# Performance work log

Measured on AMD Instinct MI355X. Metric: run time of the kernel, lower is better.

The kernel has to match this reference:

```python
import jax, jax.numpy as jnp
import numpy as np

H = 128          # hidden_size
IN = 93          # input_size
NL = 4           # num_layers
B, T = 256, 512  # batch, seq_len


def setup_inputs() -> dict:
    key = jax.random.key(0)
    ks = jax.random.split(key, 8)
    s = 1.0 / np.sqrt(H)  # pytorch LSTM init range scale
    x = jax.random.normal(ks[0], (B, T, IN), jnp.float32)
    W_ih0 = jax.random.normal(ks[1], (4 * H, IN), jnp.float32) * s   # layer 0 input weights
    W_ih_rest = jax.random.normal(ks[2], (NL - 1, 4 * H, H), jnp.float32) * s  # layers 1..3
    W_hh = jax.random.normal(ks[3], (NL, 4 * H, H), jnp.float32) * s
    b_ih = jax.random.normal(ks[4], (NL, 4 * H), jnp.float32) * s
    b_hh = jax.random.normal(ks[5], (NL, 4 * H), jnp.float32) * s
    W_fc = jax.random.normal(ks[6], (1, H), jnp.float32) * s
    b_fc = jax.random.normal(ks[7], (1,), jnp.float32) * s
    return {"x": x, "W_ih0": W_ih0, "W_ih_rest": W_ih_rest, "W_hh": W_hh,
            "b_ih": b_ih, "b_hh": b_hh, "W_fc": W_fc, "b_fc": b_fc}


def _lstm_layer(x_tm, W_ih, W_hh_l, bi, bh):
    # x_tm: [T, B, in]; precompute input-side gates as one big GEMM
    gates_x = jnp.einsum('tbi,gi->tbg', x_tm, W_ih) + bi + bh  # [T,B,4H]

    def step(carry, gx):
        h, c = carry
        g = gx + h @ W_hh_l.T                      # [B,4H]
        i, f, gg, o = jnp.split(g, 4, axis=-1)     # pytorch gate order: i,f,g,o
        i = jax.nn.sigmoid(i)
        f = jax.nn.sigmoid(f)
        gg = jnp.tanh(gg)
        o = jax.nn.sigmoid(o)
        c = f * c + i * gg
        h = o * jnp.tanh(c)
        return (h, c), h

    b = x_tm.shape[1]
    h0 = jnp.zeros((b, H), x_tm.dtype)
    (_, _), hs = jax.lax.scan(step, (h0, h0), gates_x)
    return hs  # [T,B,H]


def reference(x, W_ih0, W_ih_rest, W_hh, b_ih, b_hh, W_fc, b_fc):
    # Eval-mode forward (dropout inactive), matching model.eval() semantics.
    h = jnp.transpose(x, (1, 0, 2))  # time-major [T,B,IN]
    h = _lstm_layer(h, W_ih0, W_hh[0], b_ih[0], b_hh[0])
    for l in range(1, NL):
        h = _lstm_layer(h, W_ih_rest[l - 1], W_hh[l], b_ih[l], b_hh[l])
    out = jax.nn.sigmoid(jnp.einsum('tbh,oh->tbo', h, W_fc) + b_fc)  # [T,B,1]
    return jnp.transpose(out, (1, 0, 2))  # [B,T,1]
```

## Files before the change

### kernel.cpp

```cpp
#include <hip/hip_runtime.h>
#include <hip/hip_bf16.h>

#define H_    128
#define IN_   93
#define NL_   4
#define B_    256
#define T_    512
#define G_    512
#define W_    32
#define LOG2E 1.44269504088896f

typedef __attribute__((ext_vector_type(8))) short bf16x8;
typedef __attribute__((ext_vector_type(4))) float f32x4;
typedef unsigned long long u64;

#define RING_SLOT (B_ * H_)
#define RING_L    ((size_t)W_ * RING_SLOT)

__device__ __forceinline__ ushort bf16_rn(float f) {
    uint x = __float_as_uint(f);
    uint r = (x + 0x7FFFu + ((x >> 16) & 1u)) >> 16;
    return (ushort)r;
}
__device__ __forceinline__ float exp2_fast(float x) { return __builtin_amdgcn_exp2f(x); }
__device__ __forceinline__ float rcp_fast(float x)  { return __builtin_amdgcn_rcpf(x); }

__device__ __forceinline__ int spin_ge(int* p, int target) {
    int v = __hip_atomic_load(p, __ATOMIC_ACQUIRE, __HIP_MEMORY_SCOPE_AGENT);
    while (v < target) {
        __builtin_amdgcn_s_sleep(2);
        v = __hip_atomic_load(p, __ATOMIC_ACQUIRE, __HIP_MEMORY_SCOPE_AGENT);
    }
    return v;
}

__global__ void prep_x(const float* __restrict__ x, ushort* __restrict__ xb) {
    int idx = blockIdx.x * 256 + threadIdx.x;
    int t = idx / (B_ * 96);
    int rem = idx % (B_ * 96);
    int b = rem / 96;
    int k = rem % 96;
    float v = 0.0f;
    if (k < IN_) v = x[((size_t)b * T_ + t) * IN_ + k];
    xb[idx] = bf16_rn(v);
}

__global__ void prep_w(const float* __restrict__ Wih0,
                       const float* __restrict__ Wihr,
                       const float* __restrict__ Whh,
                       ushort* __restrict__ Wc) {
    int idx = blockIdx.x * 256 + threadIdx.x;
    int l = idx / (G_ * 256);
    int rem = idx % (G_ * 256);
    int g = rem / 256;
    int k = rem % 256;
    int kx = (l == 0) ? 96 : 128;
    float v = 0.0f;
    if (k < kx) {
        if (l == 0) { if (k < IN_) v = Wih0[g * IN_ + k]; }
        else        { v = Wihr[(((size_t)(l - 1)) * G_ + g) * H_ + k]; }
    } else if (k < kx + H_) {
        v = Whh[(((size_t)l) * G_ + g) * H_ + (k - kx)];
    }
    float scale = (g >= 256 && g < 384) ? (2.0f * LOG2E) : LOG2E;
    Wc[idx] = bf16_rn(v * scale);
}

__global__ void prep_bias(const float* __restrict__ bih,
                          const float* __restrict__ bhh,
                          float* __restrict__ bc) {
    int idx = blockIdx.x * 256 + threadIdx.x;
    int g = idx & 511;
    float scale = (g >= 256 && g < 384) ? (2.0f * LOG2E) : LOG2E;
    bc[idx] = (bih[idx] + bhh[idx]) * scale;
}

__global__ void zero_prog(int* __restrict__ prog) {
    int i = threadIdx.x;
    for (int k = i; k < NL_ * 16 * 16; k += 256) prog[k] = 0;
}

__global__ __launch_bounds__(512, 2)
void recur_all(const ushort* __restrict__ xb,
               const ushort* __restrict__ Wc,
               const float* __restrict__ biasc,
               ushort* __restrict__ ring,
               ushort* __restrict__ h3,
               int* __restrict__ prog) {
    __shared__ ushort comb[2][16][272];

    const int bid = blockIdx.x;
    const int l = bid >> 4;
    const int g = bid & 15;
    const int kx = (l == 0) ? 96 : 128;

    const int tid = threadIdx.x;
    const int w   = tid >> 6;
    const int ln  = tid & 63;
    const int q   = ln >> 4;
    const int lo  = ln & 15;
    const int u   = (w << 4) | lo;
    const int b0  = g << 4;

    const ushort* Wl = Wc + (size_t)l * G_ * 256;
    const float*  bl = biasc + l * G_;
    int* prog_self = prog + (l * 16 + g) * 16;
    int* prog_up   = prog + ((l - 1) * 16 + g) * 16;
    int* prog_down = prog + ((l + 1) * 16 + g) * 16;

    ushort* ring_self = ring + (size_t)l * RING_L;
    const ushort* ring_up = ring + (size_t)(l - 1) * RING_L;

    for (int i = tid; i < 2 * 16 * 272; i += 512) ((ushort*)comb)[i] = 0;

    bf16x8 bw[4][8];
#pragma unroll
    for (int tu = 0; tu < 4; ++tu)
#pragma unroll
        for (int s = 0; s < 8; ++s) {
            const ushort* pp = Wl + ((size_t)((tu << 7) + u) << 8) + (s << 5) + (q << 3);
            bw[tu][s] = *(const bf16x8*)pp;
        }

    const float bv0 = bl[u];
    const float bv1 = bl[128 + u];
    const float bv2 = bl[256 + u];
    const float bv3 = bl[384 + u];

    f32x4 cc = {0.0f, 0.0f, 0.0f, 0.0f};

    const int crow = tid >> 5;
    const int cu4  = (tid & 31) << 2;
    const int seg  = tid & 31;
    const bool act = (seg < 24);

    uint2 xr = {0u, 0u};
    u64 hx = 0;
    int avail = 0;

    if (l == 0) {
        if (act) xr = *(const uint2*)(xb + (size_t)(b0 + crow) * 96 + (seg << 2));
    } else {
        avail = spin_ge(prog_up, (9 < T_) ? 9 : T_);
        hx = __hip_atomic_load((u64*)(ring_up + (size_t)(b0 + crow) * H_ + cu4),
                               __ATOMIC_RELAXED, __HIP_MEMORY_SCOPE_AGENT);
    }

    __syncthreads();

    for (int t = 0; t < T_; ++t) {
        const int p = t & 1;

        if (l == 0) {
            if (act) *(uint2*)&comb[p][crow][seg << 2] = xr;
        } else {
            *(u64*)&comb[p][crow][cu4] = hx;
        }

        __syncthreads();

        if (tid == 0 && t >= 1)
            __hip_atomic_store(prog_self, t - 1, __ATOMIC_RELAXED, __HIP_MEMORY_SCOPE_AGENT);

        if (t >= 1) {
            u64 hold = *(const u64*)&comb[p][crow][kx + cu4];
            if (l < 3) {
                u64* dst = (u64*)(ring_self + (size_t)((t - 1) & (W_ - 1)) * RING_SLOT +
                                  (size_t)(b0 + crow) * H_ + cu4);
                __hip_atomic_store(dst, hold, __ATOMIC_RELAXED, __HIP_MEMORY_SCOPE_AGENT);
            } else {
                *(u64*)(h3 + (size_t)(t - 1) * RING_SLOT + (size_t)(b0 + crow) * H_ + cu4) = hold;
            }
        }

        if (l < 3 && t >= 32 && (t & 15) == 0)
            (void)spin_ge(prog_down, t - 17);

        if (t < T_ - 1) {
            if (l == 0) {
                if (act) xr = *(const uint2*)(xb + (size_t)((t + 1) * B_ + b0 + crow) * 96 + (seg << 2));
            } else {
                if (avail < t + 2) {
                    int tgt = t + 9; if (tgt > T_) tgt = T_;
                    avail = spin_ge(prog_up, tgt);
                }
                hx = __hip_atomic_load((u64*)(ring_up + (size_t)((t + 1) & (W_ - 1)) * RING_SLOT +
                                              (size_t)(b0 + crow) * H_ + cu4),
                                       __ATOMIC_RELAXED, __HIP_MEMORY_SCOPE_AGENT);
            }
        }

        f32x4 a0 = {bv0, bv0, bv0, bv0};
        f32x4 a1 = {bv1, bv1, bv1, bv1};
        f32x4 a2 = {bv2, bv2, bv2, bv2};
        f32x4 a3 = {bv3, bv3, bv3, bv3};
#pragma unroll
        for (int s = 0; s < 8; ++s) {
            bf16x8 av = *(const bf16x8*)&comb[p][lo][(s << 5) + (q << 3)];
            a0 = __builtin_amdgcn_mfma_f32_16x16x32_bf16(av, bw[0][s], a0, 0, 0, 0);
            a1 = __builtin_amdgcn_mfma_f32_16x16x32_bf16(av, bw[1][s], a1, 0, 0, 0);
            a2 = __builtin_amdgcn_mfma_f32_16x16x32_bf16(av, bw[2][s], a2, 0, 0, 0);
            a3 = __builtin_amdgcn_mfma_f32_16x16x32_bf16(av, bw[3][s], a3, 0, 0, 0);
        }

#pragma unroll
        for (int r = 0; r < 4; ++r) {
            float ei = exp2_fast(fminf(-a0[r], 60.0f));
            float ef = exp2_fast(-a1[r]);
            float eg = exp2_fast(fminf(-a2[r], 60.0f));
            float eo = exp2_fast(fminf(-a3[r], 60.0f));
            float rf  = rcp_fast(1.0f + ef);
            float rig = rcp_fast((1.0f + ei) * (1.0f + eg));
            float cn  = __builtin_fmaf(cc[r], rf, (1.0f - eg) * rig);
            cc[r] = cn;
            float ec  = exp2_fast(fminf(-2.88539008177793f * cn, 60.0f));
            float roc = rcp_fast((1.0f + eo) * (1.0f + ec));
            float h_  = (1.0f - ec) * roc;
            comb[p ^ 1][(q << 2) + r][kx + u] = bf16_rn(h_);
        }
    }

    __syncthreads();
    {
        u64 hold = *(const u64*)&comb[T_ & 1][crow][kx + cu4];
        if (l < 3) {
            u64* dst = (u64*)(ring_self + (size_t)((T_ - 1) & (W_ - 1)) * RING_SLOT +
                              (size_t)(b0 + crow) * H_ + cu4);
            __hip_atomic_store(dst, hold, __ATOMIC_RELAXED, __HIP_MEMORY_SCOPE_AGENT);
        } else {
            *(u64*)(h3 + (size_t)(T_ - 1) * RING_SLOT + (size_t)(b0 + crow) * H_ + cu4) = hold;
        }
    }
    __syncthreads();
    if (tid == 0)
        __hip_atomic_store(prog_self, T_, __ATOMIC_RELAXED, __HIP_MEMORY_SCOPE_AGENT);
}

__global__ void fc_kernel(const ushort* __restrict__ h3,
                          const float* __restrict__ wfc,
                          const float* __restrict__ bfc,
                          float* __restrict__ out) {
    int t = blockIdx.x;
    int b = threadIdx.x;
    const uint4* hp = (const uint4*)(h3 + ((size_t)t * B_ + b) * H_);
    float acc = 0.0f;
#pragma unroll
    for (int kk = 0; kk < 16; ++kk) {
        uint4 pv = hp[kk];
        const uint vv[4] = {pv.x, pv.y, pv.z, pv.w};
#pragma unroll
        for (int j = 0; j < 4; ++j) {
            float f0 = __uint_as_float(vv[j] << 16);
            float f1 = __uint_as_float(vv[j] & 0xFFFF0000u);
            acc = __builtin_fmaf(f0, wfc[kk * 8 + j * 2 + 0], acc);
            acc = __builtin_fmaf(f1, wfc[kk * 8 + j * 2 + 1], acc);
        }
    }
    float z = acc + bfc[0];
    out[(size_t)b * T_ + t] = rcp_fast(1.0f + exp2_fast(-z * LOG2E));
}

extern "C" void kernel_launch(void* const* d_in, const int* in_sizes, int n_in,
                              void* d_out, int out_size, void* d_ws, size_t ws_size,
                              hipStream_t stream) {
    const float* x    = (const float*)d_in[0];
    const float* Wih0 = (const float*)d_in[1];
    const float* Wihr = (const float*)d_in[2];
    const float* Whh  = (const float*)d_in[3];
    const float* bih  = (const float*)d_in[4];
    const float* bhh  = (const float*)d_in[5];
    const float* Wfc  = (const float*)d_in[6];
    const float* bfc  = (const float*)d_in[7];
    float* out = (float*)d_out;

    char* ws = (char*)d_ws;
    const size_t xb_bytes   = (size_t)T_ * B_ * 96 * 2;
    const size_t wc_bytes   = (size_t)NL_ * G_ * 256 * 2;
    const size_t bias_bytes = (size_t)NL_ * G_ * 4;
    const size_t prog_bytes = (size_t)NL_ * 16 * 16 * 4;
    const size_t ring_bytes = (size_t)3 * RING_L * 2;

    ushort* xb    = (ushort*)ws;
    ushort* Wc    = (ushort*)(ws + xb_bytes);
    float*  biasc = (float*)(ws + xb_bytes + wc_bytes);
    int*    prog  = (int*)(ws + xb_bytes + wc_bytes + bias_bytes);
    ushort* ring  = (ushort*)(ws + xb_bytes + wc_bytes + bias_bytes + prog_bytes);
    ushort* h3    = (ushort*)(ws + xb_bytes + wc_bytes + bias_bytes + prog_bytes + ring_bytes);

    prep_x<<<(T_ * B_ * 96) / 256, 256, 0, stream>>>(x, xb);
    prep_w<<<(NL_ * G_ * 256) / 256, 256, 0, stream>>>(Wih0, Wihr, Whh, Wc);
    prep_bias<<<(NL_ * G_) / 256, 256, 0, stream>>>(bih, bhh, biasc);
    zero_prog<<<1, 256, 0, stream>>>(prog);

    recur_all<<<NL_ * 16, 512, 0, stream>>>(xb, Wc, biasc, ring, h3, prog);

    fc_kernel<<<T_, B_, 0, stream>>>(h3, Wfc, bfc, out);
}
```

Measured before the change: 976.4 us.

## Replace spin-flag layer pipeline with chunked wavefront kernel launches and fused FC

The single persistent kernel, which chained layers through atomic progress flags and a ring buffer, is replaced by a sequence of launches. Each launch runs a 64-step time chunk, and layer l works on chunk w-l, so layers form a wavefront across launches. The h and c state is carried between launches through global buffers. The final FC plus sigmoid is fused into layer 3 using shuffles and shared memory, which removes the separate fc kernel and the h3 buffer. This drops per-step spin-waits and atomics, but adds 11 kernel launches, pipeline fill and drain bubbles, and reloads of the weight registers in every launch.

```diff
diff --git a/kernel.cpp b/kernel.cpp
--- a/kernel.cpp
+++ b/kernel.cpp
@@ -7,15 +7,18 @@
 #define B_    256
 #define T_    512
 #define G_    512
-#define W_    32
+#define C_    64
+#define NCH   (T_ / C_)
+#define NLAUNCH (NCH + NL_ - 1)
 #define LOG2E 1.44269504088896f
+
+#define STR_  260
 
 typedef __attribute__((ext_vector_type(8))) short bf16x8;
 typedef __attribute__((ext_vector_type(4))) float f32x4;
 typedef unsigned long long u64;
 
-#define RING_SLOT (B_ * H_)
-#define RING_L    ((size_t)W_ * RING_SLOT)
+#define RCHUNK ((size_t)C_ * B_ * H_)
 
 __device__ __forceinline__ ushort bf16_rn(float f) {
     uint x = __float_as_uint(f);
@@ -24,15 +27,6 @@
 }
 __device__ __forceinline__ float exp2_fast(float x) { return __builtin_amdgcn_exp2f(x); }
 __device__ __forceinline__ float rcp_fast(float x)  { return __builtin_amdgcn_rcpf(x); }
-
-__device__ __forceinline__ int spin_ge(int* p, int target) {
-    int v = __hip_atomic_load(p, __ATOMIC_ACQUIRE, __HIP_MEMORY_SCOPE_AGENT);
-    while (v < target) {
-        __builtin_amdgcn_s_sleep(2);
-        v = __hip_atomic_load(p, __ATOMIC_ACQUIRE, __HIP_MEMORY_SCOPE_AGENT);
-    }
-    return v;
-}
 
 __global__ void prep_x(const float* __restrict__ x, ushort* __restrict__ xb) {
     int idx = blockIdx.x * 256 + threadIdx.x;
@@ -75,43 +69,62 @@
     bc[idx] = (bih[idx] + bhh[idx]) * scale;
 }
 
-__global__ void zero_prog(int* __restrict__ prog) {
-    int i = threadIdx.x;
-    for (int k = i; k < NL_ * 16 * 16; k += 256) prog[k] = 0;
-}
-
 __global__ __launch_bounds__(512, 2)
-void recur_all(const ushort* __restrict__ xb,
-               const ushort* __restrict__ Wc,
-               const float* __restrict__ biasc,
-               ushort* __restrict__ ring,
-               ushort* __restrict__ h3,
-               int* __restrict__ prog) {
-    __shared__ ushort comb[2][16][272];
+void recur_chunk(const ushort* __restrict__ xb,
+                 const ushort* __restrict__ Wc,
+                 const float* __restrict__ biasc,
+                 ushort* __restrict__ ring,
+                 ushort* __restrict__ seed3,
+                 float*  __restrict__ cstate,
+                 const float* __restrict__ wfc,
+                 const float* __restrict__ bfc,
+                 float* __restrict__ out,
+                 int wlaunch) {
+    __shared__ ushort comb[2][16][STR_];
+    __shared__ float  fcbuf[2][16][8];
 
     const int bid = blockIdx.x;
     const int l = bid >> 4;
     const int g = bid & 15;
+    const int k = wlaunch - l;
+    if (k < 0 || k >= NCH) return;
+
     const int kx = (l == 0) ? 96 : 128;
+    const int t0 = k * C_;
 
     const int tid = threadIdx.x;
-    const int w   = tid >> 6;
+    const int wv  = tid >> 6;
     const int ln  = tid & 63;
     const int q   = ln >> 4;
     const int lo  = ln & 15;
-    const int u   = (w << 4) | lo;
+    const int u   = (wv << 4) | lo;
     const int b0  = g << 4;
+
+    const int crow = tid >> 5;
+    const int cu4  = (tid & 31) << 2;
+    const int seg  = tid & 31;
+    const bool act = (seg < 24);
 
     const ushort* Wl = Wc + (size_t)l * G_ * 256;
     const float*  bl = biasc + l * G_;
-    int* prog_self = prog + (l * 16 + g) * 16;
-    int* prog_up   = prog + ((l - 1) * 16 + g) * 16;
-    int* prog_down = prog + ((l + 1) * 16 + g) * 16;
-
-    ushort* ring_self = ring + (size_t)l * RING_L;
-    const ushort* ring_up = ring + (size_t)(l - 1) * RING_L;
-
-    for (int i = tid; i < 2 * 16 * 272; i += 512) ((ushort*)comb)[i] = 0;
+
+    ushort* ring_self = ring + (size_t)(2 * l + (k & 1)) * RCHUNK;
+    const ushort* ring_up = ring + (size_t)(2 * (l - 1) + (k & 1)) * RCHUNK;
+
+    for (int i = tid; i < 2 * 16 * STR_; i += 512) ((ushort*)comb)[i] = 0;
+    __syncthreads();
+
+    if (k > 0) {
+        u64 hs;
+        if (l < 3) {
+            const ushort* sp = ring + (size_t)(2 * l + ((k - 1) & 1)) * RCHUNK +
+                               (size_t)(C_ - 1) * (B_ * H_) + (size_t)(b0 + crow) * H_ + cu4;
+            hs = *(const u64*)sp;
+        } else {
+            hs = *(const u64*)(seed3 + (size_t)(b0 + crow) * H_ + cu4);
+        }
+        *(u64*)&comb[0][crow][kx + cu4] = hs;
+    }
 
     bf16x8 bw[4][8];
 #pragma unroll
@@ -126,67 +139,66 @@
     const float bv1 = bl[128 + u];
     const float bv2 = bl[256 + u];
     const float bv3 = bl[384 + u];
+    const float wfcu = wfc[u];
+    const float bfc0 = bfc[0];
 
     f32x4 cc = {0.0f, 0.0f, 0.0f, 0.0f};
-
-    const int crow = tid >> 5;
-    const int cu4  = (tid & 31) << 2;
-    const int seg  = tid & 31;
-    const bool act = (seg < 24);
-
-    uint2 xr = {0u, 0u};
-    u64 hx = 0;
-    int avail = 0;
-
+    if (k > 0) {
+#pragma unroll
+        for (int r = 0; r < 4; ++r)
+            cc[r] = cstate[(((size_t)(l * 16 + g)) * 16 + (q << 2) + r) * 128 + u];
+    }
+
+    uint2 xrc = {0u, 0u}, xrn = {0u, 0u};
+    u64 hxc = 0, hxn = 0;
     if (l == 0) {
-        if (act) xr = *(const uint2*)(xb + (size_t)(b0 + crow) * 96 + (seg << 2));
+        if (act) {
+            xrc = *(const uint2*)(xb + (size_t)((t0 + 0) * B_ + b0 + crow) * 96 + (seg << 2));
+            xrn = *(const uint2*)(xb + (size_t)((t0 + 1) * B_ + b0 + crow) * 96 + (seg << 2));
+        }
     } else {
-        avail = spin_ge(prog_up, (9 < T_) ? 9 : T_);
-        hx = __hip_atomic_load((u64*)(ring_up + (size_t)(b0 + crow) * H_ + cu4),
-                               __ATOMIC_RELAXED, __HIP_MEMORY_SCOPE_AGENT);
+        hxc = *(const u64*)(ring_up + (size_t)0 * (B_ * H_) + (size_t)(b0 + crow) * H_ + cu4);
+        hxn = *(const u64*)(ring_up + (size_t)1 * (B_ * H_) + (size_t)(b0 + crow) * H_ + cu4);
     }
 
     __syncthreads();
 
-    for (int t = 0; t < T_; ++t) {
-        const int p = t & 1;
+    for (int tl = 0; tl < C_; ++tl) {
+        const int p = tl & 1;
 
         if (l == 0) {
-            if (act) *(uint2*)&comb[p][crow][seg << 2] = xr;
+            if (act) *(uint2*)&comb[p][crow][seg << 2] = xrc;
         } else {
-            *(u64*)&comb[p][crow][cu4] = hx;
-        }
-
-        __syncthreads();
-
-        if (tid == 0 && t >= 1)
-            __hip_atomic_store(prog_self, t - 1, __ATOMIC_RELAXED, __HIP_MEMORY_SCOPE_AGENT);
-
-        if (t >= 1) {
+            *(u64*)&comb[p][crow][cu4] = hxc;
+        }
+
+        asm volatile("s_waitcnt lgkmcnt(0)" ::: "memory");
+        __builtin_amdgcn_s_barrier();
+        __builtin_amdgcn_sched_barrier(0);
+
+        if (l < 3 && tl >= 1) {
             u64 hold = *(const u64*)&comb[p][crow][kx + cu4];
-            if (l < 3) {
-                u64* dst = (u64*)(ring_self + (size_t)((t - 1) & (W_ - 1)) * RING_SLOT +
-                                  (size_t)(b0 + crow) * H_ + cu4);
-                __hip_atomic_store(dst, hold, __ATOMIC_RELAXED, __HIP_MEMORY_SCOPE_AGENT);
+            *(u64*)(ring_self + (size_t)(tl - 1) * (B_ * H_) +
+                    (size_t)(b0 + crow) * H_ + cu4) = hold;
+        }
+
+        if (l == 3 && wv == 0 && ln < 16 && tl >= 1) {
+            const float* fb = &fcbuf[(tl - 1) & 1][ln][0];
+            f32x4 s0 = *(const f32x4*)fb;
+            f32x4 s1 = *(const f32x4*)(fb + 4);
+            float s = ((s0[0] + s0[1]) + (s0[2] + s0[3])) +
+                      ((s1[0] + s1[1]) + (s1[2] + s1[3])) + bfc0;
+            out[(size_t)(b0 + ln) * T_ + (t0 + tl - 1)] =
+                rcp_fast(1.0f + exp2_fast(-s * LOG2E));
+        }
+
+        xrc = xrn; hxc = hxn;
+        if (tl + 2 < C_) {
+            if (l == 0) {
+                if (act) xrn = *(const uint2*)(xb + (size_t)((t0 + tl + 2) * B_ + b0 + crow) * 96 + (seg << 2));
             } else {
-                *(u64*)(h3 + (size_t)(t - 1) * RING_SLOT + (size_t)(b0 + crow) * H_ + cu4) = hold;
-            }
-        }
-
-        if (l < 3 && t >= 32 && (t & 15) == 0)
-            (void)spin_ge(prog_down, t - 17);
-
-        if (t < T_ - 1) {
-            if (l == 0) {
-                if (act) xr = *(const uint2*)(xb + (size_t)((t + 1) * B_ + b0 + crow) * 96 + (seg << 2));
-            } else {
-                if (avail < t + 2) {
-                    int tgt = t + 9; if (tgt > T_) tgt = T_;
-                    avail = spin_ge(prog_up, tgt);
-                }
-                hx = __hip_atomic_load((u64*)(ring_up + (size_t)((t + 1) & (W_ - 1)) * RING_SLOT +
-                                              (size_t)(b0 + crow) * H_ + cu4),
-                                       __ATOMIC_RELAXED, __HIP_MEMORY_SCOPE_AGENT);
+                hxn = *(const u64*)(ring_up + (size_t)(tl + 2) * (B_ * H_) +
+                                    (size_t)(b0 + crow) * H_ + cu4);
             }
         }
 
@@ -203,6 +215,7 @@
             a3 = __builtin_amdgcn_mfma_f32_16x16x32_bf16(av, bw[3][s], a3, 0, 0, 0);
         }
 
+        f32x4 pr;
 #pragma unroll
         for (int r = 0; r < 4; ++r) {
             float ei = exp2_fast(fminf(-a0[r], 60.0f));
@@ -217,47 +230,49 @@
             float roc = rcp_fast((1.0f + eo) * (1.0f + ec));
             float h_  = (1.0f - ec) * roc;
             comb[p ^ 1][(q << 2) + r][kx + u] = bf16_rn(h_);
-        }
-    }
-
-    __syncthreads();
+            pr[r] = h_ * wfcu;
+        }
+        if (l == 3) {
+#pragma unroll
+            for (int r = 0; r < 4; ++r) {
+                pr[r] += __shfl_xor(pr[r], 1);
+                pr[r] += __shfl_xor(pr[r], 2);
+                pr[r] += __shfl_xor(pr[r], 4);
+                pr[r] += __shfl_xor(pr[r], 8);
+            }
+            if (lo == 0) {
+#pragma unroll
+                for (int r = 0; r < 4; ++r)
+                    fcbuf[p][(q << 2) + r][wv] = pr[r];
+            }
+        }
+    }
+
+    asm volatile("s_waitcnt lgkmcnt(0)" ::: "memory");
+    __builtin_amdgcn_s_barrier();
+    __builtin_amdgcn_sched_barrier(0);
+
     {
-        u64 hold = *(const u64*)&comb[T_ & 1][crow][kx + cu4];
+        u64 hold = *(const u64*)&comb[C_ & 1][crow][kx + cu4];
         if (l < 3) {
-            u64* dst = (u64*)(ring_self + (size_t)((T_ - 1) & (W_ - 1)) * RING_SLOT +
-                              (size_t)(b0 + crow) * H_ + cu4);
-            __hip_atomic_store(dst, hold, __ATOMIC_RELAXED, __HIP_MEMORY_SCOPE_AGENT);
+            *(u64*)(ring_self + (size_t)(C_ - 1) * (B_ * H_) +
+                    (size_t)(b0 + crow) * H_ + cu4) = hold;
         } else {
-            *(u64*)(h3 + (size_t)(T_ - 1) * RING_SLOT + (size_t)(b0 + crow) * H_ + cu4) = hold;
-        }
-    }
-    __syncthreads();
-    if (tid == 0)
-        __hip_atomic_store(prog_self, T_, __ATOMIC_RELAXED, __HIP_MEMORY_SCOPE_AGENT);
-}
-
-__global__ void fc_kernel(const ushort* __restrict__ h3,
-                          const float* __restrict__ wfc,
-                          const float* __restrict__ bfc,
-                          float* __restrict__ out) {
-    int t = blockIdx.x;
-    int b = threadIdx.x;
-    const uint4* hp = (const uint4*)(h3 + ((size_t)t * B_ + b) * H_);
-    float acc = 0.0f;
-#pragma unroll
-    for (int kk = 0; kk < 16; ++kk) {
-        uint4 pv = hp[kk];
-        const uint vv[4] = {pv.x, pv.y, pv.z, pv.w};
-#pragma unroll
-        for (int j = 0; j < 4; ++j) {
-            float f0 = __uint_as_float(vv[j] << 16);
-            float f1 = __uint_as_float(vv[j] & 0xFFFF0000u);
-            acc = __builtin_fmaf(f0, wfc[kk * 8 + j * 2 + 0], acc);
-            acc = __builtin_fmaf(f1, wfc[kk * 8 + j * 2 + 1], acc);
-        }
-    }
-    float z = acc + bfc[0];
-    out[(size_t)b * T_ + t] = rcp_fast(1.0f + exp2_fast(-z * LOG2E));
+            *(u64*)(seed3 + (size_t)(b0 + crow) * H_ + cu4) = hold;
+        }
+    }
+    if (l == 3 && wv == 0 && ln < 16) {
+        const float* fb = &fcbuf[(C_ - 1) & 1][ln][0];
+        f32x4 s0 = *(const f32x4*)fb;
+        f32x4 s1 = *(const f32x4*)(fb + 4);
+        float s = ((s0[0] + s0[1]) + (s0[2] + s0[3])) +
+                  ((s1[0] + s1[1]) + (s1[2] + s1[3])) + bfc0;
+        out[(size_t)(b0 + ln) * T_ + (t0 + C_ - 1)] =
+            rcp_fast(1.0f + exp2_fast(-s * LOG2E));
+    }
+#pragma unroll
+    for (int r = 0; r < 4; ++r)
+        cstate[(((size_t)(l * 16 + g)) * 16 + (q << 2) + r) * 128 + u] = cc[r];
 }
 
 extern "C" void kernel_launch(void* const* d_in, const int* in_sizes, int n_in,
@@ -274,25 +289,25 @@
     float* out = (float*)d_out;
 
     char* ws = (char*)d_ws;
-    const size_t xb_bytes   = (size_t)T_ * B_ * 96 * 2;
-    const size_t wc_bytes   = (size_t)NL_ * G_ * 256 * 2;
-    const size_t bias_bytes = (size_t)NL_ * G_ * 4;
-    const size_t prog_bytes = (size_t)NL_ * 16 * 16 * 4;
-    const size_t ring_bytes = (size_t)3 * RING_L * 2;
+    const size_t xb_bytes    = (size_t)T_ * B_ * 96 * 2;
+    const size_t wc_bytes    = (size_t)NL_ * G_ * 256 * 2;
+    const size_t bias_bytes  = (size_t)NL_ * G_ * 4;
+    const size_t ring_bytes  = (size_t)6 * RCHUNK * 2;
+    const size_t seed3_bytes = (size_t)B_ * H_ * 2;
 
     ushort* xb    = (ushort*)ws;
     ushort* Wc    = (ushort*)(ws + xb_bytes);
     float*  biasc = (float*)(ws + xb_bytes + wc_bytes);
-    int*    prog  = (int*)(ws + xb_bytes + wc_bytes + bias_bytes);
-    ushort* ring  = (ushort*)(ws + xb_bytes + wc_bytes + bias_bytes + prog_bytes);
-    ushort* h3    = (ushort*)(ws + xb_bytes + wc_bytes + bias_bytes + prog_bytes + ring_bytes);
+    ushort* ring  = (ushort*)(ws + xb_bytes + wc_bytes + bias_bytes);
+    ushort* seed3 = (ushort*)(ws + xb_bytes + wc_bytes + bias_bytes + ring_bytes);
+    float*  cstate= (float*)(ws + xb_bytes + wc_bytes + bias_bytes + ring_bytes + seed3_bytes);
 
     prep_x<<<(T_ * B_ * 96) / 256, 256, 0, stream>>>(x, xb);
     prep_w<<<(NL_ * G_ * 256) / 256, 256, 0, stream>>>(Wih0, Wihr, Whh, Wc);
     prep_bias<<<(NL_ * G_) / 256, 256, 0, stream>>>(bih, bhh, biasc);
-    zero_prog<<<1, 256, 0, stream>>>(prog);
-
-    recur_all<<<NL_ * 16, 512, 0, stream>>>(xb, Wc, biasc, ring, h3, prog);
-
-    fc_kernel<<<T_, B_, 0, stream>>>(h3, Wfc, bfc, out);
-}
+
+    for (int w = 0; w < NLAUNCH; ++w) {
+        recur_chunk<<<NL_ * 16, 512, 0, stream>>>(xb, Wc, biasc, ring, seed3,
+                                                  cstate, Wfc, bfc, out, w);
+    }
+}
```

Result: slower. 1.175 ms (+20.4%).
